# Kernel optimization log

Measured on AMD Instinct MI355X. Metric: run time of the kernel, lower is better.

## Reference

```python
import jax, jax.numpy as jnp
import numpy as np

DIM = 128       # pair channel dim
HID = 128       # orign_dim (projection dim)
N = 384         # sequence length (square pair map)
B = 1
EPS = 1e-5


def layer_norm(x, w, b):
    m = jnp.mean(x, axis=-1, keepdims=True)
    v = jnp.mean(jnp.square(x - m), axis=-1, keepdims=True)
    return (x - m) * jax.lax.rsqrt(v + EPS) * w + b


def setup_inputs() -> dict:
    key = jax.random.key(0)
    ks = jax.random.split(key, 16)
    s = 0.02
    return {
        "x": jax.random.normal(ks[0], (B, N, N, DIM), jnp.float32),
        "norm_w": jnp.ones((DIM,), jnp.float32),
        "norm_b": jnp.zeros((DIM,), jnp.float32),
        "left_w": jax.random.normal(ks[1], (HID, DIM), jnp.float32) * s,
        "left_b": jnp.zeros((HID,), jnp.float32),
        "right_w": jax.random.normal(ks[2], (HID, DIM), jnp.float32) * s,
        "right_b": jnp.zeros((HID,), jnp.float32),
        # gates: module inits weight=0, bias=1; use small random weights + bias 1
        # to keep the same math while exercising nontrivial values
        "lgate_w": jax.random.normal(ks[3], (HID, DIM), jnp.float32) * s,
        "lgate_b": jnp.ones((HID,), jnp.float32),
        "rgate_w": jax.random.normal(ks[4], (HID, DIM), jnp.float32) * s,
        "rgate_b": jnp.ones((HID,), jnp.float32),
        "ogate_w": jax.random.normal(ks[5], (HID, DIM), jnp.float32) * s,
        "ogate_b": jnp.ones((HID,), jnp.float32),
        "ton_w": jnp.ones((HID,), jnp.float32),
        "ton_b": jnp.zeros((HID,), jnp.float32),
        "out_w": jax.random.normal(ks[6], (DIM, HID), jnp.float32) * s,
        "out_b": jnp.zeros((DIM,), jnp.float32),
    }


def reference(x, norm_w, norm_b, left_w, left_b, right_w, right_b,
              lgate_w, lgate_b, rgate_w, rgate_b, ogate_w, ogate_b,
              ton_w, ton_b, out_w, out_b):
    xn = layer_norm(x, norm_w, norm_b)                       # [B,N,N,D]
    lin = lambda w, b: jnp.einsum('bijd,ed->bije', xn, w) + b
    left = lin(left_w, left_b) * jax.nn.sigmoid(lin(lgate_w, lgate_b))
    right = lin(right_w, right_b) * jax.nn.sigmoid(lin(rgate_w, rgate_b))
    out_gate = jax.nn.sigmoid(lin(ogate_w, ogate_b))
    # ingoing mix: '... k j d, ... k i d -> ... i j d'
    out = jnp.einsum('bkjd,bkid->bijd', left, right)         # [B,N,N,H]
    out = layer_norm(out, ton_w, ton_b)
    out = jnp.einsum('bijh,dh->bijd', out, out_w) + out_b
    return out * out_gate
```

## Files before the change

kernel.cpp:

```cpp
#include <hip/hip_runtime.h>
#include <stdint.h>

typedef unsigned short u16;
typedef short bf16x8 __attribute__((ext_vector_type(8)));
typedef short bf16x4 __attribute__((ext_vector_type(4)));
typedef float f32x4 __attribute__((ext_vector_type(4)));

#define NN 384
#define DIMC 128
#define NPOS (NN*NN)
#define EPSV 1e-5f
#define LNS 136

__device__ __forceinline__ u16 f2b(float f){
  union { float f; uint32_t u; } v; v.f = f;
  return (u16)((v.u + 0x7FFFu + ((v.u >> 16) & 1u)) >> 16);
}
__device__ __forceinline__ float b2f(u16 h){
  union { uint32_t u; float f; } v; v.u = ((uint32_t)h) << 16;
  return v.f;
}
__device__ __forceinline__ float sigm(float z){
  return __builtin_amdgcn_rcpf(1.0f + __expf(-z));
}

__device__ __forceinline__ void glds16(const u16* g, u16* l){
  __builtin_amdgcn_global_load_lds((const __attribute__((address_space(1))) void*)(g),
                                   (__attribute__((address_space(3))) void*)(l), 16, 0, 0);
}

__global__ void wconv_k(const float* __restrict__ s0, const float* __restrict__ s1,
                        const float* __restrict__ s2, const float* __restrict__ s3,
                        const float* __restrict__ s4, const float* __restrict__ s5,
                        u16* __restrict__ dst){
  int bid = blockIdx.x;
  int m = bid >> 6;
  int off = ((bid & 63) << 8) + threadIdx.x;
  const float* src = s0;
  if (m==1) src=s1; else if (m==2) src=s2; else if (m==3) src=s3;
  else if (m==4) src=s4; else if (m==5) src=s5;
  dst[(m<<14) + off] = f2b(src[off]);
}

__global__ __launch_bounds__(512) void proj_k(
    const float* __restrict__ x, const float* __restrict__ nw, const float* __restrict__ nb,
    const u16* __restrict__ wb,
    const float* __restrict__ left_b, const float* __restrict__ lgate_b,
    const float* __restrict__ right_b, const float* __restrict__ rgate_b,
    const float* __restrict__ ogate_b,
    u16* __restrict__ Lp, u16* __restrict__ Rp, u16* __restrict__ gate)
{
  __shared__ u16 xn[128*LNS];
  const int tid = threadIdx.x, lane = tid & 63, wid = tid >> 6;
  const int ph = wid >> 2, wq = wid & 3;
  const int bid = blockIdx.x;
  const int c = bid % NN, r0 = (bid / NN) * 128;
  const int l15 = lane & 15, lg = lane >> 4;

  {
    float4 w0 = *(const float4*)(nw + l15*8);
    float4 w1 = *(const float4*)(nw + l15*8 + 4);
    float4 bb0 = *(const float4*)(nb + l15*8);
    float4 bb1 = *(const float4*)(nb + l15*8 + 4);
    float4 v0[4], v1[4];
    #pragma unroll
    for (int it = 0; it < 4; ++it){
      int p = ph*64 + wq*16 + it*4 + lg;
      const float* xp = x + ((size_t)(r0 + p)*NN + c)*DIMC + l15*8;
      v0[it] = *(const float4*)xp;
      v1[it] = *(const float4*)(xp + 4);
    }
    #pragma unroll
    for (int it = 0; it < 4; ++it){
      int p = ph*64 + wq*16 + it*4 + lg;
      float s  = (v0[it].x+v0[it].y)+(v0[it].z+v0[it].w)+((v1[it].x+v1[it].y)+(v1[it].z+v1[it].w));
      float sq = v0[it].x*v0[it].x+v0[it].y*v0[it].y+v0[it].z*v0[it].z+v0[it].w*v0[it].w
               + v1[it].x*v1[it].x+v1[it].y*v1[it].y+v1[it].z*v1[it].z+v1[it].w*v1[it].w;
      #pragma unroll
      for (int o = 8; o; o >>= 1){ s += __shfl_xor(s, o); sq += __shfl_xor(sq, o); }
      float mean = s * (1.0f/128.0f);
      float var  = sq * (1.0f/128.0f) - mean*mean;
      float inv  = rsqrtf(var + EPSV);
      bf16x8 o8;
      o8[0] = (short)f2b((v0[it].x - mean)*inv*w0.x + bb0.x);
      o8[1] = (short)f2b((v0[it].y - mean)*inv*w0.y + bb0.y);
      o8[2] = (short)f2b((v0[it].z - mean)*inv*w0.z + bb0.z);
      o8[3] = (short)f2b((v0[it].w - mean)*inv*w0.w + bb0.w);
      o8[4] = (short)f2b((v1[it].x - mean)*inv*w1.x + bb1.x);
      o8[5] = (short)f2b((v1[it].y - mean)*inv*w1.y + bb1.y);
      o8[6] = (short)f2b((v1[it].z - mean)*inv*w1.z + bb1.z);
      o8[7] = (short)f2b((v1[it].w - mean)*inv*w1.w + bb1.w);
      *(bf16x8*)(xn + p*LNS + l15*8) = o8;
    }
  }
  __syncthreads();

  const int kofs = lg * 8;
  const int wrow = (wq*32 + l15) * 128;
  const int xrowbase = (ph*64 + l15) * LNS;

  #pragma unroll
  for (int pr = 0; pr < 2; ++pr){
    const u16* wV = wb + (pr*2 + 0)*16384;
    const u16* wG = wb + (pr*2 + 1)*16384;
    const float* bV = pr ? right_b : left_b;
    const float* bG = pr ? rgate_b : lgate_b;
    u16* dst = pr ? Rp : Lp;

    f32x4 aV[2][4], aG[2][4];
    #pragma unroll
    for (int n = 0; n < 2; ++n)
      #pragma unroll
      for (int pt = 0; pt < 4; ++pt){ aV[n][pt] = {0.f,0.f,0.f,0.f}; aG[n][pt] = {0.f,0.f,0.f,0.f}; }

    #pragma unroll
    for (int ks = 0; ks < 4; ++ks){
      bf16x8 xf[4];
      #pragma unroll
      for (int pt = 0; pt < 4; ++pt)
        xf[pt] = *(const bf16x8*)(xn + xrowbase + pt*16*LNS + ks*32 + kofs);
      #pragma unroll
      for (int n = 0; n < 2; ++n){
        bf16x8 wv = *(const bf16x8*)(wV + wrow + n*16*128 + ks*32 + kofs);
        bf16x8 wg = *(const bf16x8*)(wG + wrow + n*16*128 + ks*32 + kofs);
        #pragma unroll
        for (int pt = 0; pt < 4; ++pt){
          aV[n][pt] = __builtin_amdgcn_mfma_f32_16x16x32_bf16(wv, xf[pt], aV[n][pt], 0, 0, 0);
          aG[n][pt] = __builtin_amdgcn_mfma_f32_16x16x32_bf16(wg, xf[pt], aG[n][pt], 0, 0, 0);
        }
      }
    }
    #pragma unroll
    for (int n = 0; n < 2; ++n){
      int ebase = wq*32 + n*16 + lg*4;
      float4 bv4 = *(const float4*)(bV + ebase);
      float4 bg4 = *(const float4*)(bG + ebase);
      #pragma unroll
      for (int r = 0; r < 4; ++r){
        float bv = r==0?bv4.x : r==1?bv4.y : r==2?bv4.z : bv4.w;
        float bg = r==0?bg4.x : r==1?bg4.y : r==2?bg4.z : bg4.w;
        u16* base = dst + (size_t)(ebase + r)*NPOS + (size_t)c*NN + r0 + ph*64 + l15;
        #pragma unroll
        for (int pt = 0; pt < 4; ++pt){
          float v = (aV[n][pt][r] + bv) * sigm(aG[n][pt][r] + bg);
          base[pt*16] = f2b(v);
        }
      }
    }
  }

  {
    const u16* wO = wb + 4*16384;
    f32x4 aO[2][4];
    #pragma unroll
    for (int n = 0; n < 2; ++n)
      #pragma unroll
      for (int pt = 0; pt < 4; ++pt) aO[n][pt] = {0.f,0.f,0.f,0.f};

    #pragma unroll
    for (int ks = 0; ks < 4; ++ks){
      bf16x8 xf[4];
      #pragma unroll
      for (int pt = 0; pt < 4; ++pt)
        xf[pt] = *(const bf16x8*)(xn + xrowbase + pt*16*LNS + ks*32 + kofs);
      #pragma unroll
      for (int n = 0; n < 2; ++n){
        bf16x8 wo = *(const bf16x8*)(wO + wrow + n*16*128 + ks*32 + kofs);
        #pragma unroll
        for (int pt = 0; pt < 4; ++pt)
          aO[n][pt] = __builtin_amdgcn_mfma_f32_16x16x32_bf16(wo, xf[pt], aO[n][pt], 0, 0, 0);
      }
    }
    #pragma unroll
    for (int n = 0; n < 2; ++n){
      int ebase = wq*32 + n*16 + lg*4;
      float4 bo4 = *(const float4*)(ogate_b + ebase);
      #pragma unroll
      for (int r = 0; r < 4; ++r){
        float bo = r==0?bo4.x : r==1?bo4.y : r==2?bo4.z : bo4.w;
        u16* base = gate + (size_t)(ebase + r)*NPOS + (size_t)c*NN + r0 + ph*64 + l15;
        #pragma unroll
        for (int pt = 0; pt < 4; ++pt)
          base[pt*16] = f2b(sigm(aO[n][pt][r] + bo));
      }
    }
  }
}

__global__ __launch_bounds__(256) void phase2_k(const u16* __restrict__ Rp, const u16* __restrict__ Lp,
                                                u16* __restrict__ outp){
  __shared__ u16 lds[17408];
  u16* At = lds;
  u16* Bt = lds + 8192;
  const int tid = threadIdx.x, lane = tid & 63, wid = tid >> 6;
  const int bid = blockIdx.x;
  const int d = bid / 9, tile = bid % 9;
  const int i0 = (tile/3)*128, j0 = (tile%3)*128;
  const int wm = wid >> 1, wn = wid & 1;
  const int jw = wm*64, iw = wn*64;
  const int l15 = lane & 15, lg = lane >> 4;
  const int rmask = l15 & 7;

  int srcoff[4];
  #pragma unroll
  for (int cc = 0; cc < 4; ++cc){
    int idx = wid*256 + cc*64 + lane;
    int row = idx >> 3, slot = idx & 7;
    srcoff[cc] = row*NN + ((slot ^ (row & 7)) * 8);
  }

  f32x4 acc[4][4];
  #pragma unroll
  for (int m = 0; m < 4; ++m)
    #pragma unroll
    for (int n = 0; n < 4; ++n) acc[m][n] = {0.f,0.f,0.f,0.f};

  const u16* Lt0 = Lp + (size_t)d*NPOS + (size_t)j0*NN;
  const u16* Rt0 = Rp + (size_t)d*NPOS + (size_t)i0*NN;

  for (int k0 = 0; k0 < NN; k0 += 64){
    __syncthreads();
    #pragma unroll
    for (int cc = 0; cc < 4; ++cc){
      glds16(Lt0 + k0 + srcoff[cc], At + (wid*4 + cc)*512);
      glds16(Rt0 + k0 + srcoff[cc], Bt + (wid*4 + cc)*512);
    }
    asm volatile("s_waitcnt vmcnt(0)" ::: "memory");
    __syncthreads();
    #pragma unroll
    for (int ks = 0; ks < 2; ++ks){
      int sl = ((ks*4 + lg) ^ rmask) * 8;
      bf16x8 af[4], bfr[4];
      #pragma unroll
      for (int m = 0; m < 4; ++m)
        af[m] = *(const bf16x8*)(At + (jw + m*16 + l15)*64 + sl);
      #pragma unroll
      for (int n = 0; n < 4; ++n)
        bfr[n] = *(const bf16x8*)(Bt + (iw + n*16 + l15)*64 + sl);
      #pragma unroll
      for (int m = 0; m < 4; ++m)
        #pragma unroll
        for (int n = 0; n < 4; ++n)
          acc[m][n] = __builtin_amdgcn_mfma_f32_16x16x32_bf16(af[m], bfr[n], acc[m][n], 0, 0, 0);
    }
  }

  __syncthreads();
  #pragma unroll
  for (int m = 0; m < 4; ++m)
    #pragma unroll
    for (int n = 0; n < 4; ++n)
      #pragma unroll
      for (int r = 0; r < 4; ++r)
        lds[(jw + m*16 + lg*4 + r)*136 + iw + n*16 + l15] = f2b(acc[m][n][r]);
  __syncthreads();
  u16* ob = outp + (size_t)d*NPOS;
  #pragma unroll
  for (int it = 0; it < 8; ++it){
    int idx = tid + it*256;
    int jl = idx >> 4, s = idx & 15;
    *(bf16x8*)(ob + (size_t)(j0 + jl)*NN + i0 + s*8) = *(const bf16x8*)(lds + jl*136 + s*8);
  }
}

__global__ __launch_bounds__(256) void phase3_k(const u16* __restrict__ outp,
    const float* __restrict__ tonw, const float* __restrict__ tonb,
    const u16* __restrict__ wOut, const float* __restrict__ out_b,
    const u16* __restrict__ gate, float* __restrict__ out)
{
  __shared__ u16 xn2[64*132];
  __shared__ float reds[4][64], redq[4][64];
  __shared__ float marr[64], iarr[64];
  const int tid = threadIdx.x, lane = tid & 63, wid = tid >> 6;
  const int bid = blockIdx.x;
  const int j = bid % NN, i0 = (bid / NN) * 64;
  const int l15 = lane & 15, lg = lane >> 4;

  float rv[32];
  float s = 0.f, sq = 0.f;
  #pragma unroll
  for (int q = 0; q < 32; ++q){
    int h = wid*32 + q;
    float v = b2f(outp[(size_t)h*NPOS + (size_t)j*NN + i0 + lane]);
    rv[q] = v; s += v; sq += v*v;
  }
  reds[wid][lane] = s; redq[wid][lane] = sq;
  __syncthreads();
  if (tid < 64){
    float ts = reds[0][tid] + reds[1][tid] + reds[2][tid] + reds[3][tid];
    float tq = redq[0][tid] + redq[1][tid] + redq[2][tid] + redq[3][tid];
    float m  = ts * (1.f/128.f);
    float var = tq * (1.f/128.f) - m*m;
    marr[tid] = m; iarr[tid] = rsqrtf(var + EPSV);
  }
  __syncthreads();
  float m = marr[lane], inv = iarr[lane];
  #pragma unroll
  for (int q = 0; q < 32; ++q){
    int h = wid*32 + q;
    float v = (rv[q] - m)*inv*tonw[h] + tonb[h];
    xn2[lane*132 + h] = f2b(v);
  }
  __syncthreads();

  f32x4 acc[8];
  #pragma unroll
  for (int n = 0; n < 8; ++n) acc[n] = {0.f,0.f,0.f,0.f};
  const int row = wid*16 + l15;
  const int kofs = lg * 8;
  #pragma unroll
  for (int ks = 0; ks < 4; ++ks){
    const u16* ap = xn2 + row*132 + ks*32 + kofs;
    bf16x4 a0 = *(const bf16x4*)ap;
    bf16x4 a1 = *(const bf16x4*)(ap + 4);
    bf16x8 af = __builtin_shufflevector(a0, a1, 0,1,2,3,4,5,6,7);
    #pragma unroll
    for (int n = 0; n < 8; ++n){
      bf16x8 bm = *(const bf16x8*)(wOut + (n*16 + l15)*128 + ks*32 + kofs);
      acc[n] = __builtin_amdgcn_mfma_f32_16x16x32_bf16(af, bm, acc[n], 0, 0, 0);
    }
  }
  #pragma unroll
  for (int n = 0; n < 8; ++n){
    int dd = n*16 + l15;
    float bo = out_b[dd];
    bf16x4 g4 = *(const bf16x4*)(gate + (size_t)dd*NPOS + (size_t)j*NN + i0 + wid*16 + lg*4);
    #pragma unroll
    for (int r = 0; r < 4; ++r){
      int p = wid*16 + lg*4 + r;
      size_t base = ((size_t)(i0 + p)*NN + j)*DIMC + dd;
      out[base] = (acc[n][r] + bo) * b2f((u16)g4[r]);
    }
  }
}

extern "C" void kernel_launch(void* const* d_in, const int* in_sizes, int n_in,
                              void* d_out, int out_size, void* d_ws, size_t ws_size,
                              hipStream_t stream){
  const float* x       = (const float*)d_in[0];
  const float* norm_w  = (const float*)d_in[1];
  const float* norm_b  = (const float*)d_in[2];
  const float* left_w  = (const float*)d_in[3];
  const float* left_b  = (const float*)d_in[4];
  const float* right_w = (const float*)d_in[5];
  const float* right_b = (const float*)d_in[6];
  const float* lgate_w = (const float*)d_in[7];
  const float* lgate_b = (const float*)d_in[8];
  const float* rgate_w = (const float*)d_in[9];
  const float* rgate_b = (const float*)d_in[10];
  const float* ogate_w = (const float*)d_in[11];
  const float* ogate_b = (const float*)d_in[12];
  const float* ton_w   = (const float*)d_in[13];
  const float* ton_b   = (const float*)d_in[14];
  const float* out_w   = (const float*)d_in[15];
  const float* out_b   = (const float*)d_in[16];

  char* ws = (char*)d_ws;
  const size_t SZ = (size_t)NPOS * DIMC * sizeof(u16);
  u16* Lp   = (u16*)(ws);
  u16* Rp   = (u16*)(ws + SZ);
  u16* gate = (u16*)(ws + 2*SZ);
  u16* outp = (u16*)(ws + 3*SZ);
  u16* wb   = (u16*)(ws + 4*SZ);

  wconv_k<<<dim3(384), dim3(256), 0, stream>>>(left_w, lgate_w, right_w, rgate_w, ogate_w, out_w, wb);
  proj_k<<<dim3(1152), dim3(512), 0, stream>>>(x, norm_w, norm_b, wb,
      left_b, lgate_b, right_b, rgate_b, ogate_b, Lp, Rp, gate);
  phase2_k<<<dim3(1152), dim3(256), 0, stream>>>(Rp, Lp, outp);
  phase3_k<<<dim3(2304), dim3(256), 0, stream>>>(outp, ton_w, ton_b, wb + 5*16384, out_b, gate, (float*)d_out);
}
```

Baseline: 187.0 us.

## Move output-gate projection into final kernel, store normalized input instead

The output-gate GEMM and sigmoid move out of the projection kernel into the final kernel. The projection kernel now writes the layer-normed input (bf16, position-major) to workspace, and the last kernel recomputes the gate with MFMA before applying it. This swaps the channel-major gate tensor's strided scatter writes and reads for contiguous row writes and reads of the same size, at the cost of extra MFMA work in phase3. The projection kernel is also shrunk to 256 threads over 64 rows with twice the grid.

```diff
diff --git a/kernel.cpp b/kernel.cpp
--- a/kernel.cpp
+++ b/kernel.cpp
@@ -42,19 +42,17 @@
   dst[(m<<14) + off] = f2b(src[off]);
 }
 
-__global__ __launch_bounds__(512) void proj_k(
+__global__ __launch_bounds__(256) void proj_k(
     const float* __restrict__ x, const float* __restrict__ nw, const float* __restrict__ nb,
     const u16* __restrict__ wb,
     const float* __restrict__ left_b, const float* __restrict__ lgate_b,
     const float* __restrict__ right_b, const float* __restrict__ rgate_b,
-    const float* __restrict__ ogate_b,
-    u16* __restrict__ Lp, u16* __restrict__ Rp, u16* __restrict__ gate)
+    u16* __restrict__ Lp, u16* __restrict__ Rp, u16* __restrict__ xng)
 {
-  __shared__ u16 xn[128*LNS];
+  __shared__ u16 xn[64*LNS];
   const int tid = threadIdx.x, lane = tid & 63, wid = tid >> 6;
-  const int ph = wid >> 2, wq = wid & 3;
   const int bid = blockIdx.x;
-  const int c = bid % NN, r0 = (bid / NN) * 128;
+  const int c = bid % NN, r0 = (bid / NN) * 64;
   const int l15 = lane & 15, lg = lane >> 4;
 
   {
@@ -65,14 +63,14 @@
     float4 v0[4], v1[4];
     #pragma unroll
     for (int it = 0; it < 4; ++it){
-      int p = ph*64 + wq*16 + it*4 + lg;
+      int p = wid*16 + it*4 + lg;
       const float* xp = x + ((size_t)(r0 + p)*NN + c)*DIMC + l15*8;
       v0[it] = *(const float4*)xp;
       v1[it] = *(const float4*)(xp + 4);
     }
     #pragma unroll
     for (int it = 0; it < 4; ++it){
-      int p = ph*64 + wq*16 + it*4 + lg;
+      int p = wid*16 + it*4 + lg;
       float s  = (v0[it].x+v0[it].y)+(v0[it].z+v0[it].w)+((v1[it].x+v1[it].y)+(v1[it].z+v1[it].w));
       float sq = v0[it].x*v0[it].x+v0[it].y*v0[it].y+v0[it].z*v0[it].z+v0[it].w*v0[it].w
                + v1[it].x*v1[it].x+v1[it].y*v1[it].y+v1[it].z*v1[it].z+v1[it].w*v1[it].w;
@@ -95,9 +93,16 @@
   }
   __syncthreads();
 
+  #pragma unroll
+  for (int it = 0; it < 4; ++it){
+    int idx = tid + it*256;
+    int p = idx >> 4, s = idx & 15;
+    *(bf16x8*)(xng + ((size_t)c*NN + r0 + p)*DIMC + s*8) = *(const bf16x8*)(xn + p*LNS + s*8);
+  }
+
   const int kofs = lg * 8;
-  const int wrow = (wq*32 + l15) * 128;
-  const int xrowbase = (ph*64 + l15) * LNS;
+  const int wrow = (wid*32 + l15) * 128;
+  const int xrowbase = l15 * LNS;
 
   #pragma unroll
   for (int pr = 0; pr < 2; ++pr){
@@ -132,56 +137,19 @@
     }
     #pragma unroll
     for (int n = 0; n < 2; ++n){
-      int ebase = wq*32 + n*16 + lg*4;
+      int ebase = wid*32 + n*16 + lg*4;
       float4 bv4 = *(const float4*)(bV + ebase);
       float4 bg4 = *(const float4*)(bG + ebase);
       #pragma unroll
       for (int r = 0; r < 4; ++r){
         float bv = r==0?bv4.x : r==1?bv4.y : r==2?bv4.z : bv4.w;
         float bg = r==0?bg4.x : r==1?bg4.y : r==2?bg4.z : bg4.w;
-        u16* base = dst + (size_t)(ebase + r)*NPOS + (size_t)c*NN + r0 + ph*64 + l15;
+        u16* base = dst + (size_t)(ebase + r)*NPOS + (size_t)c*NN + r0 + l15;
         #pragma unroll
         for (int pt = 0; pt < 4; ++pt){
           float v = (aV[n][pt][r] + bv) * sigm(aG[n][pt][r] + bg);
           base[pt*16] = f2b(v);
         }
-      }
-    }
-  }
-
-  {
-    const u16* wO = wb + 4*16384;
-    f32x4 aO[2][4];
-    #pragma unroll
-    for (int n = 0; n < 2; ++n)
-      #pragma unroll
-      for (int pt = 0; pt < 4; ++pt) aO[n][pt] = {0.f,0.f,0.f,0.f};
-
-    #pragma unroll
-    for (int ks = 0; ks < 4; ++ks){
-      bf16x8 xf[4];
-      #pragma unroll
-      for (int pt = 0; pt < 4; ++pt)
-        xf[pt] = *(const bf16x8*)(xn + xrowbase + pt*16*LNS + ks*32 + kofs);
-      #pragma unroll
-      for (int n = 0; n < 2; ++n){
-        bf16x8 wo = *(const bf16x8*)(wO + wrow + n*16*128 + ks*32 + kofs);
-        #pragma unroll
-        for (int pt = 0; pt < 4; ++pt)
-          aO[n][pt] = __builtin_amdgcn_mfma_f32_16x16x32_bf16(wo, xf[pt], aO[n][pt], 0, 0, 0);
-      }
-    }
-    #pragma unroll
-    for (int n = 0; n < 2; ++n){
-      int ebase = wq*32 + n*16 + lg*4;
-      float4 bo4 = *(const float4*)(ogate_b + ebase);
-      #pragma unroll
-      for (int r = 0; r < 4; ++r){
-        float bo = r==0?bo4.x : r==1?bo4.y : r==2?bo4.z : bo4.w;
-        u16* base = gate + (size_t)(ebase + r)*NPOS + (size_t)c*NN + r0 + ph*64 + l15;
-        #pragma unroll
-        for (int pt = 0; pt < 4; ++pt)
-          base[pt*16] = f2b(sigm(aO[n][pt][r] + bo));
       }
     }
   }
@@ -266,7 +234,8 @@
 __global__ __launch_bounds__(256) void phase3_k(const u16* __restrict__ outp,
     const float* __restrict__ tonw, const float* __restrict__ tonb,
     const u16* __restrict__ wOut, const float* __restrict__ out_b,
-    const u16* __restrict__ gate, float* __restrict__ out)
+    const u16* __restrict__ xng, const u16* __restrict__ wO,
+    const float* __restrict__ ogate_b, float* __restrict__ out)
 {
   __shared__ u16 xn2[64*132];
   __shared__ float reds[4][64], redq[4][64];
@@ -303,11 +272,28 @@
   }
   __syncthreads();
 
-  f32x4 acc[8];
-  #pragma unroll
-  for (int n = 0; n < 8; ++n) acc[n] = {0.f,0.f,0.f,0.f};
   const int row = wid*16 + l15;
   const int kofs = lg * 8;
+
+  f32x4 accO[8];
+  #pragma unroll
+  for (int n = 0; n < 8; ++n) accO[n] = {0.f,0.f,0.f,0.f};
+  {
+    const u16* xrow = xng + ((size_t)j*NN + i0 + row)*DIMC;
+    #pragma unroll
+    for (int ks = 0; ks < 4; ++ks){
+      bf16x8 af = *(const bf16x8*)(xrow + ks*32 + kofs);
+      #pragma unroll
+      for (int n = 0; n < 8; ++n){
+        bf16x8 bm = *(const bf16x8*)(wO + (n*16 + l15)*128 + ks*32 + kofs);
+        accO[n] = __builtin_amdgcn_mfma_f32_16x16x32_bf16(af, bm, accO[n], 0, 0, 0);
+      }
+    }
+  }
+
+  f32x4 acc[8];
+  #pragma unroll
+  for (int n = 0; n < 8; ++n) acc[n] = {0.f,0.f,0.f,0.f};
   #pragma unroll
   for (int ks = 0; ks < 4; ++ks){
     const u16* ap = xn2 + row*132 + ks*32 + kofs;
@@ -320,16 +306,18 @@
       acc[n] = __builtin_amdgcn_mfma_f32_16x16x32_bf16(af, bm, acc[n], 0, 0, 0);
     }
   }
+
   #pragma unroll
   for (int n = 0; n < 8; ++n){
     int dd = n*16 + l15;
     float bo = out_b[dd];
-    bf16x4 g4 = *(const bf16x4*)(gate + (size_t)dd*NPOS + (size_t)j*NN + i0 + wid*16 + lg*4);
+    float bog = ogate_b[dd];
     #pragma unroll
     for (int r = 0; r < 4; ++r){
       int p = wid*16 + lg*4 + r;
       size_t base = ((size_t)(i0 + p)*NN + j)*DIMC + dd;
-      out[base] = (acc[n][r] + bo) * b2f((u16)g4[r]);
+      float g = sigm(accO[n][r] + bog);
+      out[base] = (acc[n][r] + bo) * g;
     }
   }
 }
@@ -359,13 +347,14 @@
   const size_t SZ = (size_t)NPOS * DIMC * sizeof(u16);
   u16* Lp   = (u16*)(ws);
   u16* Rp   = (u16*)(ws + SZ);
-  u16* gate = (u16*)(ws + 2*SZ);
+  u16* xng  = (u16*)(ws + 2*SZ);
   u16* outp = (u16*)(ws + 3*SZ);
   u16* wb   = (u16*)(ws + 4*SZ);
 
   wconv_k<<<dim3(384), dim3(256), 0, stream>>>(left_w, lgate_w, right_w, rgate_w, ogate_w, out_w, wb);
-  proj_k<<<dim3(1152), dim3(512), 0, stream>>>(x, norm_w, norm_b, wb,
-      left_b, lgate_b, right_b, rgate_b, ogate_b, Lp, Rp, gate);
+  proj_k<<<dim3(2304), dim3(256), 0, stream>>>(x, norm_w, norm_b, wb,
+      left_b, lgate_b, right_b, rgate_b, Lp, Rp, xng);
   phase2_k<<<dim3(1152), dim3(256), 0, stream>>>(Rp, Lp, outp);
-  phase3_k<<<dim3(2304), dim3(256), 0, stream>>>(outp, ton_w, ton_b, wb + 5*16384, out_b, gate, (float*)d_out);
-}
+  phase3_k<<<dim3(2304), dim3(256), 0, stream>>>(outp, ton_w, ton_b, wb + 5*16384, out_b,
+      xng, wb + 4*16384, ogate_b, (float*)d_out);
+}
```

Result: slower. 219.3 us (+17.2%).
